# Kernel optimization log

Hardware: AMD Instinct MI355X
Metric: run time of the kernel (lower is better)

## Reference

```python
import jax, jax.numpy as jnp
import numpy as np

EMBED_DIM = 768
NUM_HEADS = 12


def setup_inputs() -> dict:
    key = jax.random.key(0)
    ks = jax.random.split(key, 9)
    B, N, C = 16, 1024, EMBED_DIM
    std = 1.0 / np.sqrt(C)
    x = jax.random.normal(ks[0], (B, N, C), dtype=jnp.float32)
    def w(k):
        return jax.random.normal(k, (C, C), dtype=jnp.float32) * std
    def b(k):
        return jax.random.normal(k, (C,), dtype=jnp.float32) * 0.01
    return {
        "x": x,
        "Wq": w(ks[1]), "bq": b(ks[2]),
        "Wk": w(ks[3]), "bk": b(ks[4]),
        "Wv": w(ks[5]), "bv": b(ks[6]),
        "Wo": w(ks[7]), "bo": b(ks[8]),
    }


def reference(x, Wq, bq, Wk, bk, Wv, bv, Wo, bo):
    B, N, C = x.shape
    H = NUM_HEADS
    Dh = C // H
    scale = 1.0 / np.sqrt(Dh)

    q = x @ Wq + bq  # (B, N, C)
    k = x @ Wk + bk
    v = x @ Wv + bv

    # Faithful to the original: (B, N, H, Dh) -> reshape(B*H, N, Dh)
    # WITHOUT transposing, exactly as torch_mla_core does (row-major reshape).
    q2 = q.reshape(B * H, N, Dh)
    k2 = k.reshape(B * H, N, Dh)
    v2 = v.reshape(B * H, N, Dh)

    scores = jnp.einsum('gld,gmd->glm', q2, k2) * scale  # (B*H, N, N)
    attn = jax.nn.softmax(scores, axis=-1)
    ctx2 = jnp.einsum('glm,gmd->gld', attn, v2)  # (B*H, N, Dh)

    ctx = ctx2.reshape(B, H, N, Dh).transpose(0, 2, 1, 3).reshape(B, N, C)
    out = ctx @ Wo + bo
    return out
```

## Files before the change

kernel.cpp:

```cpp
#include <hip/hip_runtime.h>
#include <hip/hip_bf16.h>
#include <cstdint>
#include <cstddef>

typedef unsigned short u16;
typedef __attribute__((ext_vector_type(8))) short s8v;
typedef __attribute__((ext_vector_type(4))) float f4v;
typedef __attribute__((ext_vector_type(8))) u16 u16x8;
typedef __attribute__((ext_vector_type(4))) uint32_t u32x4;

#define AS1 __attribute__((address_space(1)))
#define AS3 __attribute__((address_space(3)))

#define BATCH 16
#define SEQ   1024
#define EMBED 768
#define HEADS 12
#define DH    64
#define MTOT  (BATCH*SEQ)

__device__ __forceinline__ u16 f2bf(float f) {
    union { float f; uint32_t u; } v; v.f = f;
    uint32_t r = v.u + 0x7fffu + ((v.u >> 16) & 1u);
    return (u16)(r >> 16);
}

__device__ __forceinline__ void gll16(const u16* g, u16* l) {
    __builtin_amdgcn_global_load_lds((AS1 void*)g, (AS3 void*)l, 16, 0, 0);
}

#define XBLOCKS 12288
__global__ void k_pack(const float* __restrict__ x, u16* __restrict__ xb, int nx,
                       const float* __restrict__ Wq, const float* __restrict__ Wk,
                       const float* __restrict__ Wv, const float* __restrict__ Wo,
                       const float* __restrict__ bq, const float* __restrict__ bk,
                       const float* __restrict__ bv,
                       u16* __restrict__ wqkvT, u16* __restrict__ woT,
                       float* __restrict__ bqkv)
{
    if (blockIdx.x < XBLOCKS) {
        int i = (blockIdx.x * 256 + threadIdx.x) * 4;
        if (i + 3 < nx) {
            float4 f = *(const float4*)(x + i);
            ushort4 o;
            o.x = f2bf(f.x); o.y = f2bf(f.y); o.z = f2bf(f.z); o.w = f2bf(f.w);
            *(ushort4*)(xb + i) = o;
        }
        return;
    }
    const int NQKV = 2304 * 768;
    const int NO = 768 * 768;
    int t = (blockIdx.x - XBLOCKS) * 256 + threadIdx.x;
    if (t < NQKV) {
        int n = t % 2304, k = t / 2304;
        const float* src; int nn; float sc;
        if (n < 768)       { src = Wq; nn = n;        sc = 0.125f; }
        else if (n < 1536) { src = Wk; nn = n - 768;  sc = 1.0f;   }
        else               { src = Wv; nn = n - 1536; sc = 1.0f;   }
        wqkvT[(size_t)n * 768 + k] = f2bf(src[(size_t)k * 768 + nn] * sc);
    } else if (t < NQKV + NO) {
        int t2 = t - NQKV;
        int n = t2 % 768, k = t2 / 768;
        woT[(size_t)n * 768 + k] = f2bf(Wo[(size_t)k * 768 + n]);
    } else if (t < NQKV + NO + 2304) {
        int t3 = t - NQKV - NO;
        bqkv[t3] = (t3 < 768) ? bq[t3] * 0.125f
                 : ((t3 < 1536) ? bk[t3 - 768] : bv[t3 - 1536]);
    }
}

template<int MODE>
__global__ __launch_bounds__(256) void k_gemm(
    const u16* __restrict__ A, const u16* __restrict__ BT,
    const float* __restrict__ bias,
    u16* __restrict__ oq, u16* __restrict__ okk, u16* __restrict__ ov,
    float* __restrict__ of)
{
    __shared__ __attribute__((aligned(16))) u16 As[128 * 32];
    __shared__ __attribute__((aligned(16))) u16 Bs[128 * 32];
    const int tid = threadIdx.x;
    const int m0 = blockIdx.x * 128;
    const int n0 = blockIdx.y * 128;
    const int wv = tid >> 6;
    const int ln = tid & 63;
    const int l15 = ln & 15, quad = ln >> 4;
    const int wm = (wv >> 1) * 64, wn = (wv & 1) * 64;
    const int r = tid >> 2, c8 = (tid & 3) * 8;

    const u16* gA0 = A + (size_t)(m0 + r) * 768 + c8;
    const u16* gA1 = gA0 + 64 * 768;
    const u16* gB0 = BT + (size_t)(n0 + r) * 768 + c8;
    const u16* gB1 = gB0 + 64 * 768;
    u16* lA0 = As + wv * 512;
    u16* lA1 = As + 2048 + wv * 512;
    u16* lB0 = Bs + wv * 512;
    u16* lB1 = Bs + 2048 + wv * 512;

    f4v acc[4][4] = {};

    for (int kt = 0; kt < 24; ++kt) {
        const int ko = kt * 32;
        gll16(gA0 + ko, lA0);
        gll16(gA1 + ko, lA1);
        gll16(gB0 + ko, lB0);
        gll16(gB1 + ko, lB1);
        __syncthreads();
        s8v aF[4], bF[4];
#pragma unroll
        for (int i = 0; i < 4; ++i)
            aF[i] = *(const s8v*)(As + (wm + i * 16 + l15) * 32 + quad * 8);
#pragma unroll
        for (int j = 0; j < 4; ++j)
            bF[j] = *(const s8v*)(Bs + (wn + j * 16 + l15) * 32 + quad * 8);
#pragma unroll
        for (int i = 0; i < 4; ++i)
#pragma unroll
            for (int j = 0; j < 4; ++j)
                acc[i][j] = __builtin_amdgcn_mfma_f32_16x16x32_bf16(aF[i], bF[j], acc[i][j], 0, 0, 0);
        __syncthreads();
    }

#pragma unroll
    for (int j = 0; j < 4; ++j) {
        int n = n0 + wn + j * 16 + l15;
        float bs = bias[n];
        if (MODE == 0) {
            u16* dst; int nn;
            if (n < 768)       { dst = oq;  nn = n; }
            else if (n < 1536) { dst = okk; nn = n - 768; }
            else               { dst = ov;  nn = n - 1536; }
#pragma unroll
            for (int i = 0; i < 4; ++i) {
                int mrow = m0 + wm + i * 16 + quad * 4;
#pragma unroll
                for (int rg = 0; rg < 4; ++rg)
                    dst[(size_t)(mrow + rg) * 768 + nn] = f2bf(acc[i][j][rg] + bs);
            }
        } else {
#pragma unroll
            for (int i = 0; i < 4; ++i) {
                int mrow = m0 + wm + i * 16 + quad * 4;
#pragma unroll
                for (int rg = 0; rg < 4; ++rg)
                    of[(size_t)(mrow + rg) * 768 + n] = acc[i][j][rg] + bs;
            }
        }
    }
}

__global__ void k_transpose_v(const u16* __restrict__ v, u16* __restrict__ vt) {
    __shared__ __attribute__((aligned(16))) u16 ts[64 * 80];
    int g = blockIdx.x >> 4;
    int l0 = (blockIdx.x & 15) << 6;
    const u16* vg = v + (size_t)g * 65536;
    u16* vtg = vt + (size_t)g * 65536;
    int tid = threadIdx.x;
#pragma unroll
    for (int c = tid; c < 512; c += 256) {
        int l = c >> 3, d0 = (c & 7) * 8;
        *(uint4*)(ts + l * 80 + d0) = *(const uint4*)(vg + (size_t)(l0 + l) * 64 + d0);
    }
    __syncthreads();
#pragma unroll
    for (int c = tid; c < 512; c += 256) {
        int d = c >> 3, lc = (c & 7) * 8;
        u16x8 tv;
#pragma unroll
        for (int i = 0; i < 8; ++i) tv[i] = ts[(lc + i) * 80 + d];
        *(u16x8*)(vtg + (size_t)d * 1024 + l0 + lc) = tv;
    }
}

#define KS2(r_, c_) ( ((r_) << 6) + (((((c_) >> 3) ^ ((r_) & 7)) & 7) << 3) + ((c_) & 7) )

__global__ __launch_bounds__(256) void k_attn(
    const u16* __restrict__ qb, const u16* __restrict__ kb,
    const u16* __restrict__ vt, u16* __restrict__ ctx)
{
    __shared__ __attribute__((aligned(16))) u16 Ks[128 * 64];
    __shared__ __attribute__((aligned(16))) u16 Vts[64 * 136];

    const int g = blockIdx.x >> 4;
    const int q0 = (blockIdx.x & 15) << 6;
    const int tid = threadIdx.x, wv = tid >> 6;
    const int ln = tid & 63, l15 = ln & 15, quad = ln >> 4;
    const u16* qg = qb + (size_t)g * 65536;
    const u16* kg = kb + (size_t)g * 65536;
    const u16* vtg = vt + (size_t)g * 65536;

    const int krr = tid >> 3, kcb = (tid & 7) * 8;
    const int vd = tid >> 4, vc0 = (tid & 15) * 8;
    const u16* kgp = kg + (size_t)krr * 64 + kcb;
    const u16* vgp = vtg + (size_t)vd * 1024 + vc0;

    uint4 kr0 = *(const uint4*)(kgp);
    uint4 kr1 = *(const uint4*)(kgp + 2048);
    uint4 kr2 = *(const uint4*)(kgp + 4096);
    uint4 kr3 = *(const uint4*)(kgp + 6144);
    uint4 vr0 = *(const uint4*)(vgp);
    uint4 vr1 = *(const uint4*)(vgp + 16384);
    uint4 vr2 = *(const uint4*)(vgp + 32768);
    uint4 vr3 = *(const uint4*)(vgp + 49152);

    const u16* qrow = qg + (size_t)(q0 + wv * 16 + l15) * 64 + quad * 8;
    s8v aQ0 = *(const s8v*)qrow;
    s8v aQ1 = *(const s8v*)(qrow + 32);

    f4v o[4] = {};
    float rsum = 0.f;

    for (int jt = 0; jt < 8; ++jt) {
        __builtin_amdgcn_s_barrier();
        __builtin_amdgcn_sched_barrier(0);

        *(uint4*)(Ks + KS2(krr,      kcb)) = kr0;
        *(uint4*)(Ks + KS2(krr + 32, kcb)) = kr1;
        *(uint4*)(Ks + KS2(krr + 64, kcb)) = kr2;
        *(uint4*)(Ks + KS2(krr + 96, kcb)) = kr3;
        *(uint4*)(Vts + (vd     ) * 136 + vc0) = vr0;
        *(uint4*)(Vts + (vd + 16) * 136 + vc0) = vr1;
        *(uint4*)(Vts + (vd + 32) * 136 + vc0) = vr2;
        *(uint4*)(Vts + (vd + 48) * 136 + vc0) = vr3;

        if (jt < 7) {
            const size_t koff = (size_t)(jt + 1) * 8192;
            const int voff = (jt + 1) * 128;
            kr0 = *(const uint4*)(kgp + koff);
            kr1 = *(const uint4*)(kgp + koff + 2048);
            kr2 = *(const uint4*)(kgp + koff + 4096);
            kr3 = *(const uint4*)(kgp + koff + 6144);
            vr0 = *(const uint4*)(vgp + voff);
            vr1 = *(const uint4*)(vgp + voff + 16384);
            vr2 = *(const uint4*)(vgp + voff + 32768);
            vr3 = *(const uint4*)(vgp + voff + 49152);
        }

        asm volatile("s_waitcnt lgkmcnt(0)" ::: "memory");
        __builtin_amdgcn_s_barrier();
        __builtin_amdgcn_sched_barrier(0);

        f4v s[8];
        __builtin_amdgcn_s_setprio(1);
#pragma unroll
        for (int ns = 0; ns < 8; ++ns) {
            int rK = ns * 16 + l15;
            s8v b0 = *(const s8v*)(Ks + KS2(rK, quad * 8));
            s8v b1 = *(const s8v*)(Ks + KS2(rK, quad * 8 + 32));
            f4v t = {};
            t = __builtin_amdgcn_mfma_f32_16x16x32_bf16(b0, aQ0, t, 0, 0, 0);
            t = __builtin_amdgcn_mfma_f32_16x16x32_bf16(b1, aQ1, t, 0, 0, 0);
            s[ns] = t;
        }
        __builtin_amdgcn_s_setprio(0);

#pragma unroll
        for (int ns = 0; ns < 8; ++ns)
#pragma unroll
            for (int rg = 0; rg < 4; ++rg) {
                float p = __expf(s[ns][rg]);
                s[ns][rg] = p;
                rsum += p;
            }

        __builtin_amdgcn_s_setprio(1);
#pragma unroll
        for (int ks = 0; ks < 4; ++ks) {
            uint32_t a0, a1, c0, c1;
            asm("v_cvt_pk_bf16_f32 %0, %1, %2" : "=v"(a0) : "v"(s[2*ks][0]),   "v"(s[2*ks][1]));
            asm("v_cvt_pk_bf16_f32 %0, %1, %2" : "=v"(a1) : "v"(s[2*ks][2]),   "v"(s[2*ks][3]));
            asm("v_cvt_pk_bf16_f32 %0, %1, %2" : "=v"(c0) : "v"(s[2*ks+1][0]), "v"(s[2*ks+1][1]));
            asm("v_cvt_pk_bf16_f32 %0, %1, %2" : "=v"(c1) : "v"(s[2*ks+1][2]), "v"(s[2*ks+1][3]));
            asm("v_permlane32_swap_b32 %0, %1" : "+v"(a0), "+v"(c0));
            asm("v_permlane16_swap_b32 %0, %1" : "+v"(a0), "+v"(c0));
            asm("v_permlane32_swap_b32 %0, %1" : "+v"(a1), "+v"(c1));
            asm("v_permlane16_swap_b32 %0, %1" : "+v"(a1), "+v"(c1));
            u32x4 pk; pk.x = a0; pk.y = a1; pk.z = c0; pk.w = c1;
            s8v aP = __builtin_bit_cast(s8v, pk);
#pragma unroll
            for (int ds = 0; ds < 4; ++ds) {
                s8v bV = *(const s8v*)(Vts + (ds * 16 + l15) * 136 + ks * 32 + quad * 8);
                o[ds] = __builtin_amdgcn_mfma_f32_16x16x32_bf16(aP, bV, o[ds], 0, 0, 0);
            }
        }
        __builtin_amdgcn_s_setprio(0);
    }

    rsum += __shfl_xor(rsum, 16, 64);
    rsum += __shfl_xor(rsum, 32, 64);

    const int b = g / 12, h = g % 12;
    u16* cbase = ctx + (size_t)b * 786432 + h * 64;
#pragma unroll
    for (int rg = 0; rg < 4; ++rg) {
        float rs = __shfl(rsum, 20 * quad + rg, 64);
        float inv = 1.0f / rs;
        int row = q0 + wv * 16 + quad * 4 + rg;
#pragma unroll
        for (int ds = 0; ds < 4; ++ds)
            cbase[(size_t)row * 768 + ds * 16 + l15] = f2bf(o[ds][rg] * inv);
    }
}

extern "C" void kernel_launch(void* const* d_in, const int* in_sizes, int n_in,
                              void* d_out, int out_size, void* d_ws, size_t ws_size,
                              hipStream_t stream) {
    const float* x  = (const float*)d_in[0];
    const float* Wq = (const float*)d_in[1];
    const float* bq = (const float*)d_in[2];
    const float* Wk = (const float*)d_in[3];
    const float* bk = (const float*)d_in[4];
    const float* Wv = (const float*)d_in[5];
    const float* bv = (const float*)d_in[6];
    const float* Wo = (const float*)d_in[7];
    const float* bo = (const float*)d_in[8];
    float* out = (float*)d_out;

    const size_t NTOK = (size_t)MTOT * EMBED;
    char* w = (char*)d_ws;
    u16* xb    = (u16*)w;              w += NTOK * 2;
    u16* qb    = (u16*)w;              w += NTOK * 2;
    u16* kb    = (u16*)w;              w += NTOK * 2;
    u16* vb    = (u16*)w;              w += NTOK * 2;
    u16* vtb   = (u16*)w;              w += NTOK * 2;
    u16* wqkvT = (u16*)w;              w += (size_t)2304 * 768 * 2;
    u16* woT   = (u16*)w;              w += (size_t)768 * 768 * 2;
    float* bqkv = (float*)w;           w += 2304 * 4;
    u16* ctx = xb;

    k_pack<<<XBLOCKS + 9225, 256, 0, stream>>>(x, xb, (int)NTOK,
        Wq, Wk, Wv, Wo, bq, bk, bv, wqkvT, woT, bqkv);

    dim3 g1(128, 18);
    k_gemm<0><<<g1, 256, 0, stream>>>(xb, wqkvT, bqkv, qb, kb, vb, nullptr);

    k_transpose_v<<<3072, 256, 0, stream>>>(vb, vtb);
    k_attn<<<3072, 256, 0, stream>>>(qb, kb, vtb, ctx);

    dim3 g2(128, 6);
    k_gemm<1><<<g2, 256, 0, stream>>>(ctx, woT, bo, nullptr, nullptr, nullptr, out);
}
```

Before: 331.1 us.

## Double attention query tile per block and tile weight transpose through LDS

```diff
diff --git a/kernel.cpp b/kernel.cpp
--- a/kernel.cpp
+++ b/kernel.cpp
@@ -30,6 +30,7 @@
 }
 
 #define XBLOCKS 12288
+#define TBLOCKS 576
 __global__ void k_pack(const float* __restrict__ x, u16* __restrict__ xb, int nx,
                        const float* __restrict__ Wq, const float* __restrict__ Wk,
                        const float* __restrict__ Wv, const float* __restrict__ Wo,
@@ -38,8 +39,10 @@
                        u16* __restrict__ wqkvT, u16* __restrict__ woT,
                        float* __restrict__ bqkv)
 {
+    __shared__ __attribute__((aligned(16))) u16 ts[64 * 80];
+    const int tid = threadIdx.x;
     if (blockIdx.x < XBLOCKS) {
-        int i = (blockIdx.x * 256 + threadIdx.x) * 4;
+        int i = (blockIdx.x * 256 + tid) * 4;
         if (i + 3 < nx) {
             float4 f = *(const float4*)(x + i);
             ushort4 o;
@@ -48,22 +51,40 @@
         }
         return;
     }
-    const int NQKV = 2304 * 768;
-    const int NO = 768 * 768;
-    int t = (blockIdx.x - XBLOCKS) * 256 + threadIdx.x;
-    if (t < NQKV) {
-        int n = t % 2304, k = t / 2304;
-        const float* src; int nn; float sc;
-        if (n < 768)       { src = Wq; nn = n;        sc = 0.125f; }
-        else if (n < 1536) { src = Wk; nn = n - 768;  sc = 1.0f;   }
-        else               { src = Wv; nn = n - 1536; sc = 1.0f;   }
-        wqkvT[(size_t)n * 768 + k] = f2bf(src[(size_t)k * 768 + nn] * sc);
-    } else if (t < NQKV + NO) {
-        int t2 = t - NQKV;
-        int n = t2 % 768, k = t2 / 768;
-        woT[(size_t)n * 768 + k] = f2bf(Wo[(size_t)k * 768 + n]);
-    } else if (t < NQKV + NO + 2304) {
-        int t3 = t - NQKV - NO;
+    int tb = blockIdx.x - XBLOCKS;
+    if (tb < TBLOCKS) {
+        const float* src; u16* dst; int n0, k0, nn0; float sc;
+        if (tb < 432) {
+            int nt = tb % 36, kt = tb / 36;
+            n0 = nt * 64; k0 = kt * 64; dst = wqkvT;
+            if (n0 < 768)       { src = Wq; nn0 = n0;        sc = 0.125f; }
+            else if (n0 < 1536) { src = Wk; nn0 = n0 - 768;  sc = 1.0f;   }
+            else                { src = Wv; nn0 = n0 - 1536; sc = 1.0f;   }
+        } else {
+            int tb2 = tb - 432;
+            int nt = tb2 % 12, kt = tb2 / 12;
+            n0 = nt * 64; k0 = kt * 64; nn0 = n0; sc = 1.0f;
+            src = Wo; dst = woT;
+        }
+        const int r = tid >> 2, cb = (tid & 3) * 16;
+#pragma unroll
+        for (int i = 0; i < 4; ++i) {
+            float4 f = *(const float4*)(src + (size_t)(k0 + r) * 768 + nn0 + cb + i * 4);
+            ts[(cb + i * 4 + 0) * 80 + r] = f2bf(f.x * sc);
+            ts[(cb + i * 4 + 1) * 80 + r] = f2bf(f.y * sc);
+            ts[(cb + i * 4 + 2) * 80 + r] = f2bf(f.z * sc);
+            ts[(cb + i * 4 + 3) * 80 + r] = f2bf(f.w * sc);
+        }
+        __syncthreads();
+#pragma unroll
+        for (int j = 0; j < 2; ++j) {
+            u16x8 tv = *(const u16x8*)(ts + r * 80 + cb + j * 8);
+            *(u16x8*)(dst + (size_t)(n0 + r) * 768 + k0 + cb + j * 8) = tv;
+        }
+        return;
+    }
+    int t3 = (tb - TBLOCKS) * 256 + tid;
+    if (t3 < 2304) {
         bqkv[t3] = (t3 < 768) ? bq[t3] * 0.125f
                  : ((t3 < 1536) ? bk[t3 - 768] : bv[t3 - 1536]);
     }
@@ -180,8 +201,8 @@
     __shared__ __attribute__((aligned(16))) u16 Ks[128 * 64];
     __shared__ __attribute__((aligned(16))) u16 Vts[64 * 136];
 
-    const int g = blockIdx.x >> 4;
-    const int q0 = (blockIdx.x & 15) << 6;
+    const int g = blockIdx.x >> 3;
+    const int q0 = (blockIdx.x & 7) << 7;
     const int tid = threadIdx.x, wv = tid >> 6;
     const int ln = tid & 63, l15 = ln & 15, quad = ln >> 4;
     const u16* qg = qb + (size_t)g * 65536;
@@ -202,12 +223,14 @@
     uint4 vr2 = *(const uint4*)(vgp + 32768);
     uint4 vr3 = *(const uint4*)(vgp + 49152);
 
-    const u16* qrow = qg + (size_t)(q0 + wv * 16 + l15) * 64 + quad * 8;
-    s8v aQ0 = *(const s8v*)qrow;
-    s8v aQ1 = *(const s8v*)(qrow + 32);
-
-    f4v o[4] = {};
-    float rsum = 0.f;
+    const u16* qrow = qg + (size_t)(q0 + wv * 32 + l15) * 64 + quad * 8;
+    s8v aQ00 = *(const s8v*)qrow;
+    s8v aQ01 = *(const s8v*)(qrow + 32);
+    s8v aQ10 = *(const s8v*)(qrow + 1024);
+    s8v aQ11 = *(const s8v*)(qrow + 1024 + 32);
+
+    f4v o0[4] = {}, o1[4] = {};
+    float rsum0 = 0.f, rsum1 = 0.f;
 
     for (int jt = 0; jt < 8; ++jt) {
         __builtin_amdgcn_s_barrier();
@@ -239,65 +262,101 @@
         __builtin_amdgcn_s_barrier();
         __builtin_amdgcn_sched_barrier(0);
 
-        f4v s[8];
+        f4v s0[8], s1[8];
         __builtin_amdgcn_s_setprio(1);
 #pragma unroll
         for (int ns = 0; ns < 8; ++ns) {
             int rK = ns * 16 + l15;
             s8v b0 = *(const s8v*)(Ks + KS2(rK, quad * 8));
             s8v b1 = *(const s8v*)(Ks + KS2(rK, quad * 8 + 32));
-            f4v t = {};
-            t = __builtin_amdgcn_mfma_f32_16x16x32_bf16(b0, aQ0, t, 0, 0, 0);
-            t = __builtin_amdgcn_mfma_f32_16x16x32_bf16(b1, aQ1, t, 0, 0, 0);
-            s[ns] = t;
+            f4v t0 = {};
+            t0 = __builtin_amdgcn_mfma_f32_16x16x32_bf16(b0, aQ00, t0, 0, 0, 0);
+            t0 = __builtin_amdgcn_mfma_f32_16x16x32_bf16(b1, aQ01, t0, 0, 0, 0);
+            s0[ns] = t0;
+            f4v t1 = {};
+            t1 = __builtin_amdgcn_mfma_f32_16x16x32_bf16(b0, aQ10, t1, 0, 0, 0);
+            t1 = __builtin_amdgcn_mfma_f32_16x16x32_bf16(b1, aQ11, t1, 0, 0, 0);
+            s1[ns] = t1;
         }
         __builtin_amdgcn_s_setprio(0);
 
+        s8v aP0[4], aP1[4];
 #pragma unroll
         for (int ns = 0; ns < 8; ++ns)
 #pragma unroll
             for (int rg = 0; rg < 4; ++rg) {
-                float p = __expf(s[ns][rg]);
-                s[ns][rg] = p;
-                rsum += p;
+                float p = __expf(s0[ns][rg]);
+                s0[ns][rg] = p;
+                rsum0 += p;
             }
-
-        __builtin_amdgcn_s_setprio(1);
 #pragma unroll
         for (int ks = 0; ks < 4; ++ks) {
             uint32_t a0, a1, c0, c1;
-            asm("v_cvt_pk_bf16_f32 %0, %1, %2" : "=v"(a0) : "v"(s[2*ks][0]),   "v"(s[2*ks][1]));
-            asm("v_cvt_pk_bf16_f32 %0, %1, %2" : "=v"(a1) : "v"(s[2*ks][2]),   "v"(s[2*ks][3]));
-            asm("v_cvt_pk_bf16_f32 %0, %1, %2" : "=v"(c0) : "v"(s[2*ks+1][0]), "v"(s[2*ks+1][1]));
-            asm("v_cvt_pk_bf16_f32 %0, %1, %2" : "=v"(c1) : "v"(s[2*ks+1][2]), "v"(s[2*ks+1][3]));
+            asm("v_cvt_pk_bf16_f32 %0, %1, %2" : "=v"(a0) : "v"(s0[2*ks][0]),   "v"(s0[2*ks][1]));
+            asm("v_cvt_pk_bf16_f32 %0, %1, %2" : "=v"(a1) : "v"(s0[2*ks][2]),   "v"(s0[2*ks][3]));
+            asm("v_cvt_pk_bf16_f32 %0, %1, %2" : "=v"(c0) : "v"(s0[2*ks+1][0]), "v"(s0[2*ks+1][1]));
+            asm("v_cvt_pk_bf16_f32 %0, %1, %2" : "=v"(c1) : "v"(s0[2*ks+1][2]), "v"(s0[2*ks+1][3]));
             asm("v_permlane32_swap_b32 %0, %1" : "+v"(a0), "+v"(c0));
             asm("v_permlane16_swap_b32 %0, %1" : "+v"(a0), "+v"(c0));
             asm("v_permlane32_swap_b32 %0, %1" : "+v"(a1), "+v"(c1));
             asm("v_permlane16_swap_b32 %0, %1" : "+v"(a1), "+v"(c1));
             u32x4 pk; pk.x = a0; pk.y = a1; pk.z = c0; pk.w = c1;
-            s8v aP = __builtin_bit_cast(s8v, pk);
+            aP0[ks] = __builtin_bit_cast(s8v, pk);
+        }
+#pragma unroll
+        for (int ns = 0; ns < 8; ++ns)
+#pragma unroll
+            for (int rg = 0; rg < 4; ++rg) {
+                float p = __expf(s1[ns][rg]);
+                s1[ns][rg] = p;
+                rsum1 += p;
+            }
+#pragma unroll
+        for (int ks = 0; ks < 4; ++ks) {
+            uint32_t a0, a1, c0, c1;
+            asm("v_cvt_pk_bf16_f32 %0, %1, %2" : "=v"(a0) : "v"(s1[2*ks][0]),   "v"(s1[2*ks][1]));
+            asm("v_cvt_pk_bf16_f32 %0, %1, %2" : "=v"(a1) : "v"(s1[2*ks][2]),   "v"(s1[2*ks][3]));
+            asm("v_cvt_pk_bf16_f32 %0, %1, %2" : "=v"(c0) : "v"(s1[2*ks+1][0]), "v"(s1[2*ks+1][1]));
+            asm("v_cvt_pk_bf16_f32 %0, %1, %2" : "=v"(c1) : "v"(s1[2*ks+1][2]), "v"(s1[2*ks+1][3]));
+            asm("v_permlane32_swap_b32 %0, %1" : "+v"(a0), "+v"(c0));
+            asm("v_permlane16_swap_b32 %0, %1" : "+v"(a0), "+v"(c0));
+            asm("v_permlane32_swap_b32 %0, %1" : "+v"(a1), "+v"(c1));
+            asm("v_permlane16_swap_b32 %0, %1" : "+v"(a1), "+v"(c1));
+            u32x4 pk; pk.x = a0; pk.y = a1; pk.z = c0; pk.w = c1;
+            aP1[ks] = __builtin_bit_cast(s8v, pk);
+        }
+
+        __builtin_amdgcn_s_setprio(1);
+#pragma unroll
+        for (int ks = 0; ks < 4; ++ks)
 #pragma unroll
             for (int ds = 0; ds < 4; ++ds) {
                 s8v bV = *(const s8v*)(Vts + (ds * 16 + l15) * 136 + ks * 32 + quad * 8);
-                o[ds] = __builtin_amdgcn_mfma_f32_16x16x32_bf16(aP, bV, o[ds], 0, 0, 0);
+                o0[ds] = __builtin_amdgcn_mfma_f32_16x16x32_bf16(aP0[ks], bV, o0[ds], 0, 0, 0);
+                o1[ds] = __builtin_amdgcn_mfma_f32_16x16x32_bf16(aP1[ks], bV, o1[ds], 0, 0, 0);
             }
-        }
         __builtin_amdgcn_s_setprio(0);
     }
 
-    rsum += __shfl_xor(rsum, 16, 64);
-    rsum += __shfl_xor(rsum, 32, 64);
+    rsum0 += __shfl_xor(rsum0, 16, 64);
+    rsum0 += __shfl_xor(rsum0, 32, 64);
+    rsum1 += __shfl_xor(rsum1, 16, 64);
+    rsum1 += __shfl_xor(rsum1, 32, 64);
 
     const int b = g / 12, h = g % 12;
     u16* cbase = ctx + (size_t)b * 786432 + h * 64;
 #pragma unroll
     for (int rg = 0; rg < 4; ++rg) {
-        float rs = __shfl(rsum, 20 * quad + rg, 64);
-        float inv = 1.0f / rs;
-        int row = q0 + wv * 16 + quad * 4 + rg;
+        int row0 = q0 + wv * 32 + quad * 4 + rg;
+        float inv0 = 1.0f / __shfl(rsum0, 20 * quad + rg, 64);
 #pragma unroll
         for (int ds = 0; ds < 4; ++ds)
-            cbase[(size_t)row * 768 + ds * 16 + l15] = f2bf(o[ds][rg] * inv);
+            cbase[(size_t)row0 * 768 + ds * 16 + l15] = f2bf(o0[ds][rg] * inv0);
+        int row1 = row0 + 16;
+        float inv1 = 1.0f / __shfl(rsum1, 20 * quad + rg, 64);
+#pragma unroll
+        for (int ds = 0; ds < 4; ++ds)
+            cbase[(size_t)row1 * 768 + ds * 16 + l15] = f2bf(o1[ds][rg] * inv1);
     }
 }
 
@@ -327,14 +386,14 @@
     float* bqkv = (float*)w;           w += 2304 * 4;
     u16* ctx = xb;
 
-    k_pack<<<XBLOCKS + 9225, 256, 0, stream>>>(x, xb, (int)NTOK,
+    k_pack<<<XBLOCKS + TBLOCKS + 9, 256, 0, stream>>>(x, xb, (int)NTOK,
         Wq, Wk, Wv, Wo, bq, bk, bv, wqkvT, woT, bqkv);
 
     dim3 g1(128, 18);
     k_gemm<0><<<g1, 256, 0, stream>>>(xb, wqkvT, bqkv, qb, kb, vb, nullptr);
 
     k_transpose_v<<<3072, 256, 0, stream>>>(vb, vtb);
-    k_attn<<<3072, 256, 0, stream>>>(qb, kb, vtb, ctx);
+    k_attn<<<1536, 256, 0, stream>>>(qb, kb, vtb, ctx);
 
     dim3 g2(128, 6);
     k_gemm<1><<<g2, 256, 0, stream>>>(ctx, woT, bo, nullptr, nullptr, nullptr, out);
```

After: 321.8 us. -2.8%, faster.
